# Kernel tuning notes

Hardware: AMD Instinct MI355X
Metric: run time of the kernel (lower is better)

Reference implementation:

```python
import jax, jax.numpy as jnp
import numpy as np

B, S, DIM = 2, 2048, 2048
H, KVH, HD = 16, 4, 128
G = H // KVH  # GQA groups = 4
THETA = 10000.0


def setup_inputs() -> dict:
    key = jax.random.key(0)
    k0, k1, k2, k3, k4 = jax.random.split(key, 5)
    x = jax.random.normal(k0, (B, S, DIM), jnp.float32)
    # RoPE table: [max_seq_len, head_dim//2, 2] holding (cos, sin)
    inv_freq = 1.0 / (THETA ** (jnp.arange(0, HD, 2, dtype=jnp.float32) / HD))
    angles = jnp.outer(jnp.arange(S, dtype=jnp.float32), inv_freq)  # [S, HD//2]
    freqs_cis = jnp.stack([jnp.cos(angles), jnp.sin(angles)], axis=-1)
    sc = 0.02
    wq = jax.random.normal(k1, (H * HD, DIM), jnp.float32) * sc
    wk = jax.random.normal(k2, (KVH * HD, DIM), jnp.float32) * sc
    wv = jax.random.normal(k3, (KVH * HD, DIM), jnp.float32) * sc
    wo = jax.random.normal(k4, (DIM, H * HD), jnp.float32) * sc
    return {"x": x, "freqs_cis": freqs_cis, "wq": wq, "wk": wk, "wv": wv, "wo": wo}


def apply_rope(x, freqs_cis):
    # x: [B, S, h, HD]; freqs_cis: [max_S, HD//2, 2]
    s = x.shape[1]
    xr = x.astype(jnp.float32).reshape(*x.shape[:-1], -1, 2)  # [B,S,h,HD//2,2]
    cos = freqs_cis[:s, :, 0][None, :, None, :]  # [1,S,1,HD//2]
    sin = freqs_cis[:s, :, 1][None, :, None, :]
    x0, x1 = xr[..., 0], xr[..., 1]
    out = jnp.stack([x0 * cos - x1 * sin, x0 * sin + x1 * cos], axis=-1)
    return out.reshape(x.shape).astype(x.dtype)


def reference(x, freqs_cis, wq, wk, wv, wo):
    b, s, d = x.shape
    q = (x @ wq.T).reshape(b, s, H, HD)
    k = (x @ wk.T).reshape(b, s, KVH, HD)
    v = (x @ wv.T).reshape(b, s, KVH, HD)
    q = apply_rope(q, freqs_cis)
    k = apply_rope(k, freqs_cis)
    # GQA expand: repeat_interleave along head dim
    k = jnp.repeat(k, G, axis=2)  # [b,s,H,HD]
    v = jnp.repeat(v, G, axis=2)
    q = jnp.swapaxes(q, 1, 2)  # [b,H,s,HD]
    k = jnp.swapaxes(k, 1, 2)
    v = jnp.swapaxes(v, 1, 2)
    scale = 1.0 / jnp.sqrt(jnp.asarray(HD, dtype=q.dtype))
    scores = jnp.einsum('bhqd,bhkd->bhqk', q, k) * scale  # [b,H,s,s]
    causal = jnp.tril(jnp.ones((s, s), dtype=bool))
    scores = jnp.where(causal[None, None], scores, jnp.finfo(scores.dtype).min)
    probs = jax.nn.softmax(scores, axis=-1)
    attn = jnp.einsum('bhqk,bhkd->bhqd', probs, v)  # [b,H,s,HD]
    attn = jnp.swapaxes(attn, 1, 2).reshape(b, s, H * HD)
    return attn @ wo.T
```

## Files before the change

### kernel.cpp

```cpp
#include <hip/hip_runtime.h>
#include <stdint.h>

#define B_ 2
#define S_ 2048
#define DIM_ 2048
#define H_ 16
#define KVH_ 4
#define HD_ 128

typedef short short8 __attribute__((ext_vector_type(8)));
typedef float f4 __attribute__((ext_vector_type(4)));
typedef float f16v __attribute__((ext_vector_type(16)));
typedef unsigned int uint2v __attribute__((ext_vector_type(2)));
typedef unsigned short u16;

#define KSCALE (0.08838834764831845f * 1.4426950408889634f)

__device__ __forceinline__ float bf2f(u16 u) {
    union { unsigned int i; float f; } c; c.i = ((unsigned int)u) << 16; return c.f;
}
__device__ __forceinline__ u16 f2bf(float f) {
    union { float f; unsigned int i; } c; c.f = f;
    return (u16)((c.i + 0x7fffu + ((c.i >> 16) & 1u)) >> 16);
}
__device__ __forceinline__ unsigned pk_bf16(float lo, float hi) {
    unsigned r;
    asm("v_cvt_pk_bf16_f32 %0, %1, %2" : "=v"(r) : "v"(lo), "v"(hi));
    return r;
}

#define GLDS16(gp, lp) \
    __builtin_amdgcn_global_load_lds((const __attribute__((address_space(1))) unsigned int*)(gp), \
                                     (__attribute__((address_space(3))) unsigned int*)(lp), 16, 0, 0)

__global__ void cast_all(const float* __restrict__ x,  const float* __restrict__ wq,
                         const float* __restrict__ wk, const float* __restrict__ wv,
                         const float* __restrict__ wo,
                         u16* __restrict__ xb, u16* __restrict__ wqkvb, u16* __restrict__ wob) {
    int i = blockIdx.x * 256 + threadIdx.x;
    const float4* src; ushort4* dst; int j;
    if (i < 2097152)      { src = (const float4*)x;  dst = (ushort4*)xb;                 j = i; }
    else if (i < 3145728) { src = (const float4*)wq; dst = (ushort4*)wqkvb;              j = i - 2097152; }
    else if (i < 3407872) { src = (const float4*)wk; dst = (ushort4*)wqkvb + 1048576;    j = i - 3145728; }
    else if (i < 3670016) { src = (const float4*)wv; dst = (ushort4*)wqkvb + 1310720;    j = i - 3407872; }
    else                  { src = (const float4*)wo; dst = (ushort4*)wob;                j = i - 3670016; }
    float4 v = src[j];
    ushort4 o;
    o.x = f2bf(v.x); o.y = f2bf(v.y); o.z = f2bf(v.z); o.w = f2bf(v.w);
    dst[j] = o;
}

template<bool OUT_BF16, int NBX>
__global__ __launch_bounds__(256) void gemm_bt(const u16* __restrict__ A,
                                               const u16* __restrict__ W,
                                               void* __restrict__ Cout,
                                               int M, int N, int K) {
    __shared__ u16 As[128 * 32];
    __shared__ u16 Bs[128 * 32];
    int t = threadIdx.x, lane = t & 63, w = t >> 6;
    int quad = lane >> 4, l16 = lane & 15;
    int wm = w & 1, wn = w >> 1;
    int bid = blockIdx.x;
    int xcd = bid & 7, grp = bid >> 3;
    int bx = grp % NBX, by = (grp / NBX) * 8 + xcd;
    size_t m0 = (size_t)by * 128, n0 = (size_t)bx * 128;

    int c0 = w * 2;
    int ar = c0 * 16 + (lane >> 2);
    int ac = (lane & 3) * 8;
    const u16* Abase = A + (m0 + ar) * (size_t)K + ac;
    const u16* Bbase = W + (n0 + ar) * (size_t)K + ac;
    u16* Adst = As + c0 * 512;
    u16* Bdst = Bs + c0 * 512;

    f4 acc[4][4];
    #pragma unroll
    for (int i = 0; i < 4; i++)
        #pragma unroll
        for (int j = 0; j < 4; j++) acc[i][j] = (f4){0.f, 0.f, 0.f, 0.f};

    int nk = K >> 5;
    for (int kt = 0; kt < nk; kt++) {
        const u16* ga = Abase + kt * 32;
        const u16* gb = Bbase + kt * 32;
        GLDS16(ga, Adst);
        GLDS16(ga + 16 * (size_t)K, Adst + 512);
        GLDS16(gb, Bdst);
        GLDS16(gb + 16 * (size_t)K, Bdst + 512);
        __syncthreads();
        short8 a[4], b[4];
        #pragma unroll
        for (int i = 0; i < 4; i++) a[i] = *(const short8*)&As[(wm * 64 + i * 16 + l16) * 32 + quad * 8];
        #pragma unroll
        for (int j = 0; j < 4; j++) b[j] = *(const short8*)&Bs[(wn * 64 + j * 16 + l16) * 32 + quad * 8];
        #pragma unroll
        for (int i = 0; i < 4; i++)
            #pragma unroll
            for (int j = 0; j < 4; j++)
                acc[i][j] = __builtin_amdgcn_mfma_f32_16x16x32_bf16(a[i], b[j], acc[i][j], 0, 0, 0);
        __syncthreads();
    }
    #pragma unroll
    for (int i = 0; i < 4; i++) {
        size_t row = m0 + wm * 64 + i * 16 + quad * 4;
        #pragma unroll
        for (int j = 0; j < 4; j++) {
            size_t col = n0 + wn * 64 + j * 16 + l16;
            #pragma unroll
            for (int r = 0; r < 4; r++) {
                if (OUT_BF16) ((u16*)Cout)[(row + r) * N + col] = f2bf(acc[i][j][r]);
                else          ((float*)Cout)[(row + r) * N + col] = acc[i][j][r];
            }
        }
    }
}

__global__ __launch_bounds__(256) void pack_k(const u16* __restrict__ QKV,
                                              const float* __restrict__ freqs,
                                              u16* __restrict__ Kp) {
    int gid = blockIdx.x * 256 + threadIdx.x;
    int u = gid & 15, row = (gid >> 4) & 63, kt = (gid >> 10) & 31, bk = gid >> 15;
    int b = bk >> 2, kvh = bk & 3;
    int s = kt * 64 + row;
    int d8 = u ^ (row & 7);
    const u16* src = QKV + (size_t)(b * S_ + s) * 3072 + 2048 + kvh * HD_ + d8 * 8;
    short8 v = *(const short8*)src;
    short8 o;
    #pragma unroll
    for (int jp = 0; jp < 4; jp++) {
        float2 cw = ((const float2*)freqs)[s * 64 + d8 * 4 + jp];
        float x0 = bf2f((u16)v[2 * jp]), x1 = bf2f((u16)v[2 * jp + 1]);
        o[2 * jp]     = (short)f2bf(x0 * cw.x - x1 * cw.y);
        o[2 * jp + 1] = (short)f2bf(x0 * cw.y + x1 * cw.x);
    }
    *(short8*)&Kp[(size_t)gid * 8] = o;
}

__global__ __launch_bounds__(256) void pack_v(const u16* __restrict__ QKV, u16* __restrict__ Vp) {
    __shared__ u16 L[64 * 136];
    int bid = blockIdx.x;
    int bk = bid & 7, kt = bid >> 3;
    int b = bk >> 2, kvh = bk & 3;
    int t = threadIdx.x;
    const u16* src = QKV + (size_t)(b * S_ + kt * 64) * 3072 + 2560 + kvh * HD_;
    #pragma unroll
    for (int it = 0; it < 4; it++) {
        int idx = t + it * 256;
        int r = idx >> 4, c = idx & 15;
        *(short8*)&L[r * 136 + c * 8] = *(const short8*)(src + (size_t)r * 3072 + c * 8);
    }
    __syncthreads();
    u16* dst = Vp + (size_t)(bk * 32 + kt) * 8192;
    #pragma unroll
    for (int it = 0; it < 4; it++) {
        int idx = t + it * 256;
        int hd = idx >> 3, u = idx & 7;
        int k0 = (u ^ (hd & 7)) * 8;
        short8 v;
        #pragma unroll
        for (int jj = 0; jj < 8; jj++) v[jj] = (short)L[(k0 + jj) * 136 + hd];
        *(short8*)&dst[(size_t)idx * 8] = v;
    }
}

__global__ __launch_bounds__(256) __attribute__((amdgpu_waves_per_eu(2, 2)))
void attn_kernel(const u16* __restrict__ QKV,
                 const float* __restrict__ freqs,
                 const u16* __restrict__ Kp,
                 const u16* __restrict__ Vp,
                 u16* __restrict__ Ob) {
    __shared__ u16 Ks[2][8192];
    __shared__ u16 Vs[2][8192];
    int bid = blockIdx.x;
    int jj_ = bid & 255, half = bid >> 8;
    int bk = jj_ & 7, qpr = jj_ >> 3;
    int qb = half ? qpr : 63 - qpr;
    int b = bk >> 2, kvh = bk & 3;
    int t = threadIdx.x, lane = t & 63, w = t >> 6;
    int l31 = lane & 31, hi = lane >> 5, l7 = lane & 7;
    int h = kvh * 4 + w;
    int nkt = (qb >> 1) + 1;

    short8 qf[8];
    {
        int s = qb * 32 + l31;
        const u16* qp = QKV + ((size_t)(b * S_ + s)) * 3072 + h * HD_ + hi * 8;
        const float2* fr2 = (const float2*)freqs;
        #pragma unroll
        for (int ds = 0; ds < 8; ds++) {
            short8 v = *(const short8*)(qp + ds * 16);
            short8 o;
            #pragma unroll
            for (int jp = 0; jp < 4; jp++) {
                float2 cs = fr2[s * 64 + ds * 8 + hi * 4 + jp];
                float x0 = bf2f((u16)v[2 * jp]), x1 = bf2f((u16)v[2 * jp + 1]);
                o[2 * jp]     = (short)f2bf((x0 * cs.x - x1 * cs.y) * KSCALE);
                o[2 * jp + 1] = (short)f2bf((x0 * cs.y + x1 * cs.x) * KSCALE);
            }
            qf[ds] = o;
        }
    }

    float m_i = -3e38f, ls = 0.f;
    f16v o4[4];
    #pragma unroll
    for (int i = 0; i < 4; i++)
        #pragma unroll
        for (int r = 0; r < 16; r++) o4[i][r] = 0.f;

    const u16* Kpb = Kp + (size_t)bk * 32 * 8192;
    const u16* Vpb = Vp + (size_t)bk * 32 * 8192;
    int so = w * 2048 + lane * 8;

    {
        const u16* ks = Kpb + so;
        const u16* vs = Vpb + so;
        #pragma unroll
        for (int i = 0; i < 4; i++) {
            GLDS16(ks + i * 512, &Ks[0][w * 2048 + i * 512]);
            GLDS16(vs + i * 512, &Vs[0][w * 2048 + i * 512]);
        }
    }

    for (int kt = 0; kt < nkt; kt++) {
        int buf = kt & 1;
        __syncthreads();
        if (kt + 1 < nkt) {
            int nb = buf ^ 1;
            const u16* ks = Kpb + (size_t)(kt + 1) * 8192 + so;
            const u16* vs = Vpb + (size_t)(kt + 1) * 8192 + so;
            #pragma unroll
            for (int i = 0; i < 4; i++) {
                GLDS16(ks + i * 512, &Ks[nb][w * 2048 + i * 512]);
                GLDS16(vs + i * 512, &Vs[nb][w * 2048 + i * 512]);
            }
        }

        f16v sacc[2];
        #pragma unroll
        for (int k2 = 0; k2 < 2; k2++)
            #pragma unroll
            for (int r = 0; r < 16; r++) sacc[k2][r] = 0.f;
        #pragma unroll
        for (int ds = 0; ds < 8; ds++) {
            int uK = ((ds * 2 + hi) ^ l7) * 8;
            short8 kf0 = *(const short8*)&Ks[buf][l31 * 128 + uK];
            short8 kf1 = *(const short8*)&Ks[buf][(32 + l31) * 128 + uK];
            sacc[0] = __builtin_amdgcn_mfma_f32_32x32x16_bf16(kf0, qf[ds], sacc[0], 0, 0, 0);
            sacc[1] = __builtin_amdgcn_mfma_f32_32x32x16_bf16(kf1, qf[ds], sacc[1], 0, 0, 0);
        }

        if (kt == nkt - 1) {
            int off0 = kt * 64 - qb * 32;
            #pragma unroll
            for (int k2 = 0; k2 < 2; k2++) {
                #pragma unroll
                for (int r = 0; r < 16; r++) {
                    int colo = off0 + k2 * 32 + (r & 3) + ((r >> 2) << 3) + (hi << 2);
                    if (colo > l31) sacc[k2][r] = -3e38f;
                }
            }
        }

        float pm = sacc[0][0];
        #pragma unroll
        for (int r = 1; r < 16; r++) pm = fmaxf(pm, sacc[0][r]);
        #pragma unroll
        for (int r = 0; r < 16; r++) pm = fmaxf(pm, sacc[1][r]);
        pm = fmaxf(pm, __shfl_xor(pm, 32, 64));
        if (__any(pm > m_i + 8.0f)) {
            float mnew = fmaxf(m_i, pm);
            float al = exp2f(m_i - mnew);
            ls *= al;
            #pragma unroll
            for (int i = 0; i < 4; i++)
                #pragma unroll
                for (int r = 0; r < 16; r++) o4[i][r] *= al;
            m_i = mnew;
        }

        short8 pa[4];
        #pragma unroll
        for (int k2 = 0; k2 < 2; k2++) {
            float p[16];
            #pragma unroll
            for (int r = 0; r < 16; r++) {
                p[r] = exp2f(sacc[k2][r] - m_i);
                ls += p[r];
            }
            unsigned W0 = pk_bf16(p[0], p[1]),   W1 = pk_bf16(p[2], p[3]);
            unsigned W2 = pk_bf16(p[4], p[5]),   W3 = pk_bf16(p[6], p[7]);
            unsigned W4 = pk_bf16(p[8], p[9]),   W5 = pk_bf16(p[10], p[11]);
            unsigned W6 = pk_bf16(p[12], p[13]), W7 = pk_bf16(p[14], p[15]);
            uint2v r02 = __builtin_amdgcn_permlane32_swap(W0, W2, false, false);
            uint2v r13 = __builtin_amdgcn_permlane32_swap(W1, W3, false, false);
            uint2v r46 = __builtin_amdgcn_permlane32_swap(W4, W6, false, false);
            uint2v r57 = __builtin_amdgcn_permlane32_swap(W5, W7, false, false);
            union { unsigned u[4]; short8 s8; } flo, fhi;
            flo.u[0] = r02[0]; flo.u[1] = r13[0]; flo.u[2] = r02[1]; flo.u[3] = r13[1];
            fhi.u[0] = r46[0]; fhi.u[1] = r57[0]; fhi.u[2] = r46[1]; fhi.u[3] = r57[1];
            pa[k2 * 2]     = flo.s8;
            pa[k2 * 2 + 1] = fhi.s8;
        }

        #pragma unroll
        for (int ks = 0; ks < 4; ks++) {
            int uV = ((ks * 2 + hi) ^ l7) * 8;
            #pragma unroll
            for (int ht = 0; ht < 4; ht++) {
                short8 vf = *(const short8*)&Vs[buf][(ht * 32 + l31) * 64 + uV];
                o4[ht] = __builtin_amdgcn_mfma_f32_32x32x16_bf16(vf, pa[ks], o4[ht], 0, 0, 0);
            }
        }
    }

    ls += __shfl_xor(ls, 32, 64);
    float rl = 1.0f / ls;
    size_t row = (size_t)b * S_ + qb * 32 + l31;
    u16* op = Ob + row * 2048 + h * HD_;
    #pragma unroll
    for (int ht = 0; ht < 4; ht++) {
        #pragma unroll
        for (int g = 0; g < 4; g++) {
            ushort4 st;
            st.x = f2bf(o4[ht][4 * g + 0] * rl);
            st.y = f2bf(o4[ht][4 * g + 1] * rl);
            st.z = f2bf(o4[ht][4 * g + 2] * rl);
            st.w = f2bf(o4[ht][4 * g + 3] * rl);
            *(ushort4*)&op[ht * 32 + g * 8 + hi * 4] = st;
        }
    }
}

extern "C" void kernel_launch(void* const* d_in, const int* in_sizes, int n_in,
                              void* d_out, int out_size, void* d_ws, size_t ws_size,
                              hipStream_t stream) {
    const float* x     = (const float*)d_in[0];
    const float* freqs = (const float*)d_in[1];
    const float* wq    = (const float*)d_in[2];
    const float* wk    = (const float*)d_in[3];
    const float* wv    = (const float*)d_in[4];
    const float* wo    = (const float*)d_in[5];
    float* out = (float*)d_out;

    char* p = (char*)d_ws;
    u16* xb    = (u16*)p; p += (size_t)4096 * 2048 * 2;
    u16* wqkvb = (u16*)p; p += (size_t)3072 * 2048 * 2;
    u16* wob   = (u16*)p; p += (size_t)2048 * 2048 * 2;
    u16* QKVb  = (u16*)p; p += (size_t)4096 * 3072 * 2;
    u16* Kpb   = (u16*)p; p += (size_t)8 * 32 * 8192 * 2;
    u16* Vpb   = (u16*)p; p += (size_t)8 * 32 * 8192 * 2;
    u16* attnb = xb;

    cast_all<<<18432, 256, 0, stream>>>(x, wq, wk, wv, wo, xb, wqkvb, wob);

    gemm_bt<true, 24><<<768, 256, 0, stream>>>(xb, wqkvb, QKVb, 4096, 3072, 2048);

    pack_k<<<1024, 256, 0, stream>>>(QKVb, freqs, Kpb);
    pack_v<<<256, 256, 0, stream>>>(QKVb, Vpb);

    attn_kernel<<<512, 256, 0, stream>>>(QKVb, freqs, Kpb, Vpb, attnb);

    gemm_bt<false, 16><<<512, 256, 0, stream>>>(attnb, wob, out, 4096, 2048, 2048);
}
```

Measured before the change: 319.9 us.

## Replace 128x128 GEMM with 256x256 double-buffered ping-pong pipelined GEMM

Replaces the single-buffered 128x128x32 GEMM with a 256x256x64 tile kernel using 512 threads, double-buffered LDS, XOR-swizzled shared layout, and staged global->LDS loads interleaved between quarter MFMA blocks with setprio. The intent is to raise arithmetic intensity per LDS load, hide global load latency, and avoid bank conflicts. Grids shrink to 192 and 128 blocks, which underfills the 256 CUs and risks lower occupancy and load imbalance.

Result: no change. 317.6 us (-0.7%).

```diff
diff --git a/kernel.cpp b/kernel.cpp
--- a/kernel.cpp
+++ b/kernel.cpp
@@ -32,6 +32,9 @@
 #define GLDS16(gp, lp) \
     __builtin_amdgcn_global_load_lds((const __attribute__((address_space(1))) unsigned int*)(gp), \
                                      (__attribute__((address_space(3))) unsigned int*)(lp), 16, 0, 0)
+
+#define BAR()     asm volatile("s_barrier" ::: "memory")
+#define WAITLGKM() asm volatile("s_waitcnt lgkmcnt(0)" ::: "memory")
 
 __global__ void cast_all(const float* __restrict__ x,  const float* __restrict__ wq,
                          const float* __restrict__ wk, const float* __restrict__ wv,
@@ -51,68 +54,106 @@
 }
 
 template<bool OUT_BF16, int NBX>
-__global__ __launch_bounds__(256) void gemm_bt(const u16* __restrict__ A,
-                                               const u16* __restrict__ W,
-                                               void* __restrict__ Cout,
-                                               int M, int N, int K) {
-    __shared__ u16 As[128 * 32];
-    __shared__ u16 Bs[128 * 32];
+__global__ __launch_bounds__(512, 2) void gemm256(const u16* __restrict__ A,
+                                                  const u16* __restrict__ W,
+                                                  void* __restrict__ Cout,
+                                                  int M, int N, int K) {
+    __shared__ u16 As[2][16384];
+    __shared__ u16 Bs[2][16384];
     int t = threadIdx.x, lane = t & 63, w = t >> 6;
-    int quad = lane >> 4, l16 = lane & 15;
-    int wm = w & 1, wn = w >> 1;
+    int quad = lane >> 4, l16 = lane & 15, l7 = lane & 7;
+    int wm = w >> 2, wn = w & 3;
     int bid = blockIdx.x;
     int xcd = bid & 7, grp = bid >> 3;
     int bx = grp % NBX, by = (grp / NBX) * 8 + xcd;
-    size_t m0 = (size_t)by * 128, n0 = (size_t)bx * 128;
-
-    int c0 = w * 2;
-    int ar = c0 * 16 + (lane >> 2);
-    int ac = (lane & 3) * 8;
-    const u16* Abase = A + (m0 + ar) * (size_t)K + ac;
-    const u16* Bbase = W + (n0 + ar) * (size_t)K + ac;
-    u16* Adst = As + c0 * 512;
-    u16* Bdst = Bs + c0 * 512;
-
-    f4 acc[4][4];
-    #pragma unroll
-    for (int i = 0; i < 4; i++)
+    size_t m0 = (size_t)by * 256, n0 = (size_t)bx * 256;
+
+    int srow = lane >> 3;
+    int sunit = (lane & 7) ^ srow;
+    int rR0a = (w >> 2) * 64 + (w & 3) * 8;
+    const u16* Ag = A + (m0 + srow) * (size_t)K + sunit * 8;
+    const u16* Bg = W + (n0 + srow) * (size_t)K + sunit * 8;
+
+#define STG_A(pl, tk, r0) GLDS16(Ag + ((size_t)((r0) + w * 8)) * K + (tk) * 64, (pl) + ((r0) + w * 8) * 64)
+#define STG_B(pl, tk, r0) GLDS16(Bg + ((size_t)((r0) + w * 8)) * K + (tk) * 64, (pl) + ((r0) + w * 8) * 64)
+#define STG_BR(pl, tk, bse) GLDS16(Bg + ((size_t)((bse) + rR0a)) * K + (tk) * 64, (pl) + ((bse) + rR0a) * 64)
+
+#define LDA(mh) { \
+    _Pragma("unroll") for (int i_ = 0; i_ < 4; i_++) \
+    _Pragma("unroll") for (int k_ = 0; k_ < 2; k_++) \
+        a[i_][k_] = *(const short8*)&pAc[(wm * 128 + (mh) * 64 + i_ * 16 + l16) * 64 + (((quad + 4 * k_) ^ l7) << 3)]; }
+#define LDB(nh) { \
+    _Pragma("unroll") for (int j_ = 0; j_ < 2; j_++) \
+    _Pragma("unroll") for (int k_ = 0; k_ < 2; k_++) \
+        b[j_][k_] = *(const short8*)&pBc[(wn * 64 + (nh) * 32 + j_ * 16 + l16) * 64 + (((quad + 4 * k_) ^ l7) << 3)]; }
+#define MFMA_Q(mh, nh) { \
+    __builtin_amdgcn_s_setprio(1); \
+    _Pragma("unroll") for (int i_ = 0; i_ < 4; i_++) \
+    _Pragma("unroll") for (int j_ = 0; j_ < 2; j_++) \
+    _Pragma("unroll") for (int k_ = 0; k_ < 2; k_++) \
+        acc[(mh) * 4 + i_][(nh) * 2 + j_] = __builtin_amdgcn_mfma_f32_16x16x32_bf16( \
+            a[i_][k_], b[j_][k_], acc[(mh) * 4 + i_][(nh) * 2 + j_], 0, 0, 0); \
+    __builtin_amdgcn_s_setprio(0); }
+
+    f4 acc[8][4];
+    #pragma unroll
+    for (int i = 0; i < 8; i++)
         #pragma unroll
         for (int j = 0; j < 4; j++) acc[i][j] = (f4){0.f, 0.f, 0.f, 0.f};
 
-    int nk = K >> 5;
-    for (int kt = 0; kt < nk; kt++) {
-        const u16* ga = Abase + kt * 32;
-        const u16* gb = Bbase + kt * 32;
-        GLDS16(ga, Adst);
-        GLDS16(ga + 16 * (size_t)K, Adst + 512);
-        GLDS16(gb, Bdst);
-        GLDS16(gb + 16 * (size_t)K, Bdst + 512);
-        __syncthreads();
-        short8 a[4], b[4];
-        #pragma unroll
-        for (int i = 0; i < 4; i++) a[i] = *(const short8*)&As[(wm * 64 + i * 16 + l16) * 32 + quad * 8];
-        #pragma unroll
-        for (int j = 0; j < 4; j++) b[j] = *(const short8*)&Bs[(wn * 64 + j * 16 + l16) * 32 + quad * 8];
-        #pragma unroll
-        for (int i = 0; i < 4; i++)
-            #pragma unroll
-            for (int j = 0; j < 4; j++)
-                acc[i][j] = __builtin_amdgcn_mfma_f32_16x16x32_bf16(a[i], b[j], acc[i][j], 0, 0, 0);
-        __syncthreads();
-    }
-    #pragma unroll
-    for (int i = 0; i < 4; i++) {
-        size_t row = m0 + wm * 64 + i * 16 + quad * 4;
+    int NT = K >> 6;
+
+    #pragma unroll
+    for (int pt = 0; pt < 2; pt++) {
+        u16* pa = &As[pt][0]; u16* pb = &Bs[pt][0];
+        #pragma unroll
+        for (int r0 = 0; r0 < 256; r0 += 64) { STG_A(pa, pt, r0); STG_B(pb, pt, r0); }
+    }
+    asm volatile("s_waitcnt vmcnt(0)" ::: "memory");
+    BAR();
+
+    short8 a[4][2], b[2][2];
+    for (int tt = 0; tt < NT; tt++) {
+        int c = tt & 1, nc = c ^ 1;
+        u16* pAc = &As[c][0];  u16* pBc = &Bs[c][0];
+        u16* pAn = &As[nc][0]; u16* pBn = &Bs[nc][0];
+        bool s1 = (tt >= 1) & (tt + 1 < NT);
+        bool s2 = (tt + 2 < NT);
+        LDA(0); LDB(0);
+        if (s1) { STG_A(pAn, tt + 1, 64); STG_A(pAn, tt + 1, 192); }
+        BAR(); WAITLGKM(); MFMA_Q(0, 0); BAR();
+        LDB(1);
+        if (s1) { STG_BR(pBn, tt + 1, 32); STG_BR(pBn, tt + 1, 160); }
+        BAR(); WAITLGKM(); MFMA_Q(0, 1); BAR();
+        LDA(1); LDB(0);
+        if (s2) { STG_A(pAc, tt + 2, 0); STG_A(pAc, tt + 2, 128); }
+        BAR(); WAITLGKM(); MFMA_Q(1, 0); BAR();
+        if (s2) asm volatile("s_waitcnt vmcnt(2)" ::: "memory");
+        else    asm volatile("s_waitcnt vmcnt(0)" ::: "memory");
+        LDB(1);
+        if (s2) { STG_BR(pBc, tt + 2, 0); STG_BR(pBc, tt + 2, 128); }
+        BAR(); WAITLGKM(); MFMA_Q(1, 1); BAR();
+    }
+
+    #pragma unroll
+    for (int i = 0; i < 8; i++) {
+        size_t row = m0 + wm * 128 + i * 16 + quad * 4;
         #pragma unroll
         for (int j = 0; j < 4; j++) {
             size_t col = n0 + wn * 64 + j * 16 + l16;
             #pragma unroll
             for (int r = 0; r < 4; r++) {
-                if (OUT_BF16) ((u16*)Cout)[(row + r) * N + col] = f2bf(acc[i][j][r]);
-                else          ((float*)Cout)[(row + r) * N + col] = acc[i][j][r];
-            }
-        }
-    }
+                if (OUT_BF16) ((u16*)Cout)[(row + r) * (size_t)N + col] = f2bf(acc[i][j][r]);
+                else          ((float*)Cout)[(row + r) * (size_t)N + col] = acc[i][j][r];
+            }
+        }
+    }
+#undef STG_A
+#undef STG_B
+#undef STG_BR
+#undef LDA
+#undef LDB
+#undef MFMA_Q
 }
 
 __global__ __launch_bounds__(256) void pack_k(const u16* __restrict__ QKV,
@@ -354,12 +395,12 @@
 
     cast_all<<<18432, 256, 0, stream>>>(x, wq, wk, wv, wo, xb, wqkvb, wob);
 
-    gemm_bt<true, 24><<<768, 256, 0, stream>>>(xb, wqkvb, QKVb, 4096, 3072, 2048);
+    gemm256<true, 12><<<192, 512, 0, stream>>>(xb, wqkvb, QKVb, 4096, 3072, 2048);
 
     pack_k<<<1024, 256, 0, stream>>>(QKVb, freqs, Kpb);
     pack_v<<<256, 256, 0, stream>>>(QKVb, Vpb);
 
     attn_kernel<<<512, 256, 0, stream>>>(QKVb, freqs, Kpb, Vpb, attnb);
 
-    gemm_bt<false, 16><<<512, 256, 0, stream>>>(attnb, wob, out, 4096, 2048, 2048);
-}
+    gemm256<false, 8><<<128, 512, 0, stream>>>(attnb, wob, out, 4096, 2048, 2048);
+}
```
